# Kernel tuning notes

Measured on AMD Instinct MI355X. Metric: run time of the kernel, lower is better.

## Reference

```python
import jax, jax.numpy as jnp
import numpy as np

B, S, HID, NH, KCLIP = 2, 1500, 1024, 16, 64
HD = HID // NH  # 64


def setup_inputs() -> dict:
    key = jax.random.key(0)
    ks = jax.random.split(key, 16)
    std = 0.02
    inp = {
        "query": jax.random.normal(ks[0], (B, S, HID), jnp.float32),
        "key": jax.random.normal(ks[1], (B, S, HID), jnp.float32),
        "value": jax.random.normal(ks[2], (B, S, HID), jnp.float32),
        # per-head projection weights, stacked over heads: [NH, HID, HD]
        "Wq": jax.random.normal(ks[3], (NH, HID, HD), jnp.float32) * std,
        "bq": jax.random.normal(ks[4], (NH, HD), jnp.float32) * std,
        "Wk": jax.random.normal(ks[5], (NH, HID, HD), jnp.float32) * std,
        "bk": jax.random.normal(ks[6], (NH, HD), jnp.float32) * std,
        "Wv": jax.random.normal(ks[7], (NH, HID, HD), jnp.float32) * std,
        "bv": jax.random.normal(ks[8], (NH, HD), jnp.float32) * std,
        # Shaw relative-position embedding tables: [2k+1, HD]
        "pe_k": jax.random.normal(ks[9], (2 * KCLIP + 1, HD), jnp.float32) * std,
        "pe_v": jax.random.normal(ks[10], (2 * KCLIP + 1, HD), jnp.float32) * std,
        # output projection (torch Linear stored as x @ W + b here)
        "W_fc": jax.random.normal(ks[11], (HID, HID), jnp.float32) * std,
        "b_fc": jax.random.normal(ks[12], (HID,), jnp.float32) * std,
    }
    return inp


def _rel_bias(pe, length, k_clip):
    idx = jnp.arange(length)
    dist = jnp.clip(idx[None, :] - idx[:, None], -k_clip, k_clip) + k_clip
    return pe[dist]  # [S, S, HD]


def reference(query, key, value, Wq, bq, Wk, bk, Wv, bv, pe_k, pe_v, W_fc, b_fc):
    head_dim = Wq.shape[-1]
    seq = query.shape[1]
    k_clip = (pe_k.shape[0] - 1) // 2

    kb = _rel_bias(pe_k, seq, k_clip)  # [S, S, HD]
    vb = _rel_bias(pe_v, seq, k_clip)  # [S, S, HD]

    # batched per-head projections: [B, NH, S, HD]
    Q = jnp.einsum('bsh,nhd->bnsd', query, Wq) + bq[None, :, None, :]
    K = jnp.einsum('bsh,nhd->bnsd', key, Wk) + bk[None, :, None, :]
    V = jnp.einsum('bsh,nhd->bnsd', value, Wv) + bv[None, :, None, :]

    # content term + Shaw relative-key bias term
    scores = jnp.einsum('bnqd,bnkd->bnqk', Q, K) \
           + jnp.einsum('bnqd,qkd->bnqk', Q, kb)
    scores = scores / jnp.sqrt(jnp.asarray(head_dim, scores.dtype))

    w = jax.nn.softmax(scores, axis=-1)  # [B, NH, S, S]

    out = jnp.einsum('bnqk,bnkd->bnqd', w, V) \
        + jnp.einsum('bnqk,qkd->bnqd', w, vb)

    # concat heads (head order matches ModuleList concatenation)
    hidden = out.transpose(0, 2, 1, 3).reshape(query.shape[0], seq, -1)
    return hidden @ W_fc + b_fc
```

## Files before the change

kernel.cpp:

```cpp
#include <hip/hip_runtime.h>
#include <math.h>

#define B_     2
#define S_     1500
#define HID_   1024
#define NH_    16
#define HD_    64
#define M_     (B_*S_)
#define SP_    1536
#define LOG2E  1.4426950408889634f

typedef short bf16x8 __attribute__((ext_vector_type(8)));
typedef short bf16x4 __attribute__((ext_vector_type(4)));
typedef float f32x4  __attribute__((ext_vector_type(4)));

__device__ __forceinline__ float b2f(short s) {
    unsigned u = ((unsigned)(unsigned short)s) << 16;
    return __uint_as_float(u);
}
__device__ __forceinline__ short f2b(float f) {
    unsigned u = __float_as_uint(f);
    unsigned r = (u + 0x7FFFu + ((u >> 16) & 1u)) >> 16;
    return (short)r;
}
__device__ __forceinline__ void gload16(const short* src, short* lds) {
    __builtin_amdgcn_global_load_lds(
        (const __attribute__((address_space(1))) void*)src,
        (__attribute__((address_space(3))) void*)lds, 16, 0, 0);
}

__global__ __launch_bounds__(256) void cvt_act3(
    const float* __restrict__ q, const float* __restrict__ k,
    const float* __restrict__ v, short* __restrict__ oq,
    short* __restrict__ ok, short* __restrict__ ov)
{
    const float* src = blockIdx.y == 0 ? q : blockIdx.y == 1 ? k : v;
    short* dst       = blockIdx.y == 0 ? oq : blockIdx.y == 1 ? ok : ov;
    int i = blockIdx.x * 256 + threadIdx.x;
    const float4* p = (const float4*)(src + (size_t)i * 8);
    float4 a = p[0], b = p[1];
    bf16x8 o;
    o[0]=f2b(a.x); o[1]=f2b(a.y); o[2]=f2b(a.z); o[3]=f2b(a.w);
    o[4]=f2b(b.x); o[5]=f2b(b.y); o[6]=f2b(b.z); o[7]=f2b(b.w);
    *(bf16x8*)(dst + (size_t)i * 8) = o;
}

__global__ __launch_bounds__(256) void prep_w(
    const float* __restrict__ Wq, const float* __restrict__ Wk,
    const float* __restrict__ Wv, const float* __restrict__ Wfc,
    const float* __restrict__ pe_k, const float* __restrict__ pe_v,
    short* __restrict__ Wqt, short* __restrict__ Wkt, short* __restrict__ Wvt,
    short* __restrict__ Wfh, short* __restrict__ Wfl,
    short* __restrict__ pe_kb, short* __restrict__ pe_vt)
{
    int z = blockIdx.x, tid = threadIdx.x;
    if (z == 1024) {
        for (int s = tid; s < 144 * 64; s += 256) {
            int j = s >> 6, d = s & 63;
            pe_kb[s] = (j < 129) ? f2b(pe_k[j * 64 + d]) : (short)0;
        }
        for (int s = tid; s < 64 * 160; s += 256) {
            int d = s / 160, j = s - d * 160;
            pe_vt[s] = (j < 129) ? f2b(pe_v[j * 64 + d]) : (short)0;
        }
        return;
    }
    __shared__ float T[64][65];
    const float* src; short* dhi; short* dlo = nullptr;
    int C, c0, r0; float scale = 1.f;
    if (z < 768) {
        int widx = z >> 8, rem = z & 255;
        int h = rem >> 4, rt = rem & 15;
        src = (widx == 0 ? Wq : widx == 1 ? Wk : Wv) + (size_t)h * 1024 * 64;
        dhi = (widx == 0 ? Wqt : widx == 1 ? Wkt : Wvt) + (size_t)h * 64 * 1024;
        scale = (widx == 0) ? 0.125f * LOG2E : 1.0f;
        C = 64; c0 = 0; r0 = rt * 64;
    } else {
        int idx = z - 768;
        src = Wfc; dhi = Wfh; dlo = Wfl;
        C = 1024; c0 = (idx >> 4) * 64; r0 = (idx & 15) * 64;
    }
#pragma unroll
    for (int i = 0; i < 4; ++i) {
        int slot = tid + i * 256;
        int r = slot >> 4, cg = (slot & 15) * 4;
        float4 v = *(const float4*)(src + (size_t)(r0 + r) * C + c0 + cg);
        T[r][cg+0] = v.x*scale; T[r][cg+1] = v.y*scale;
        T[r][cg+2] = v.z*scale; T[r][cg+3] = v.w*scale;
    }
    __syncthreads();
#pragma unroll
    for (int i = 0; i < 16; ++i) {
        int slot = tid + i * 256;
        int c = slot >> 6, r = slot & 63;
        float v = T[r][c];
        short hi = f2b(v);
        size_t o = (size_t)(c0 + c) * 1024 + r0 + r;
        dhi[o] = hi;
        if (dlo) dlo[o] = f2b(v - b2f(hi));
    }
}

__device__ __forceinline__ void gemm_core(
    const short* __restrict__ Ahi, const short* __restrict__ Alo,
    const short* __restrict__ Bhi, const short* __restrict__ Blo,
    int kIters, int m0, int n0, short* As, short* Bs, f32x4 (&acc)[4][4])
{
    const int tid = threadIdx.x, w = tid >> 6, lane = tid & 63;
    const int l15 = lane & 15, lr4 = lane >> 4;
    const int wr = w >> 1, wc = w & 1;

    for (int it = 0; it < kIters; ++it) {
        int kt = it * 64;
        int seg = kt >> 10, kk0 = kt & 1023;
        const short* Aseg = (seg == 1) ? Alo : Ahi;
        const short* Bseg = (seg == 2) ? Blo : Bhi;
        __syncthreads();
#pragma unroll
        for (int c = 0; c < 4; ++c) {
            int slot = (w * 4 + c) * 64 + lane;
            int r = slot >> 3, cb = slot & 7;
            int sm = m0 + r; sm = sm < M_ ? sm : M_ - 1;
            gload16(Aseg + (size_t)sm * 1024 + kk0 + ((cb ^ (r & 7)) * 8),
                    As + (size_t)(w * 4 + c) * 512);
            gload16(Bseg + (size_t)(n0 + r) * 1024 + kk0 + ((cb ^ (r & 7)) * 8),
                    Bs + (size_t)(w * 4 + c) * 512);
        }
        __syncthreads();
#pragma unroll
        for (int kh = 0; kh < 2; ++kh) {
            bf16x8 aF[4], bF[4];
#pragma unroll
            for (int mi = 0; mi < 4; ++mi) {
                int r = wr * 64 + mi * 16 + l15;
                aF[mi] = *(const bf16x8*)(As + r * 64 + (((kh*4+lr4) ^ (r & 7)) * 8));
            }
#pragma unroll
            for (int ni = 0; ni < 4; ++ni) {
                int r = wc * 64 + ni * 16 + l15;
                bF[ni] = *(const bf16x8*)(Bs + r * 64 + (((kh*4+lr4) ^ (r & 7)) * 8));
            }
#pragma unroll
            for (int mi = 0; mi < 4; ++mi)
#pragma unroll
                for (int ni = 0; ni < 4; ++ni)
                    acc[mi][ni] = __builtin_amdgcn_mfma_f32_16x16x32_bf16(
                        aF[mi], bF[ni], acc[mi][ni], 0, 0, 0);
        }
    }
}

__global__ __launch_bounds__(256) void gemm_qkv(
    const short* __restrict__ qb, const short* __restrict__ kb,
    const short* __restrict__ vb, const short* __restrict__ Wqt,
    const short* __restrict__ Wkt, const short* __restrict__ Wvt,
    const float* __restrict__ bq, const float* __restrict__ bk,
    const float* __restrict__ bv,
    short* __restrict__ Qp, short* __restrict__ Kp, short* __restrict__ Vp)
{
    __shared__ short As[128 * 64];
    __shared__ short Bs[128 * 64];
    const int z = blockIdx.z;
    const short* A  = z == 0 ? qb : z == 1 ? kb : vb;
    const short* Bw = z == 0 ? Wqt : z == 1 ? Wkt : Wvt;
    const float* bias = z == 0 ? bq : z == 1 ? bk : bv;
    const float bscale = z == 0 ? 0.125f * LOG2E : 1.0f;
    short* out = z == 0 ? Qp : z == 1 ? Kp : Vp;
    const int m0 = blockIdx.x * 128, n0 = blockIdx.y * 128;

    f32x4 zf = {0.f,0.f,0.f,0.f};
    f32x4 acc[4][4];
#pragma unroll
    for (int i = 0; i < 4; ++i)
#pragma unroll
        for (int j = 0; j < 4; ++j) acc[i][j] = zf;

    gemm_core(A, A, Bw, Bw, 16, m0, n0, As, Bs, acc);

    const int tid = threadIdx.x, w = tid >> 6, lane = tid & 63;
    const int l15 = lane & 15, lr4 = lane >> 4;
    const int wr = w >> 1, wc = w & 1;
#pragma unroll
    for (int mi = 0; mi < 4; ++mi)
#pragma unroll
        for (int rr = 0; rr < 4; ++rr) {
            int m = m0 + wr * 64 + mi * 16 + lr4 * 4 + rr;
            if (m >= M_) continue;
            int b = m / S_, s = m - b * S_;
#pragma unroll
            for (int ni = 0; ni < 4; ++ni) {
                int n = n0 + wc * 64 + ni * 16 + l15;
                float v = acc[mi][ni][rr] + bias[n] * bscale;
                int h = n >> 6, d = n & 63;
                out[(((size_t)(b * NH_ + h)) * S_ + s) * HD_ + d] = f2b(v);
            }
        }
}

__global__ __launch_bounds__(256) void gemm_fc(
    const short* __restrict__ Ahi, const short* __restrict__ Alo,
    const short* __restrict__ Bhi, const short* __restrict__ Blo,
    const float* __restrict__ bias, float* __restrict__ out)
{
    __shared__ short As[128 * 64];
    __shared__ short Bs[128 * 64];
    const int m0 = blockIdx.x * 128, n0 = blockIdx.y * 128;
    f32x4 zf = {0.f,0.f,0.f,0.f};
    f32x4 acc[4][4];
#pragma unroll
    for (int i = 0; i < 4; ++i)
#pragma unroll
        for (int j = 0; j < 4; ++j) acc[i][j] = zf;

    gemm_core(Ahi, Alo, Bhi, Blo, 48, m0, n0, As, Bs, acc);

    const int tid = threadIdx.x, w = tid >> 6, lane = tid & 63;
    const int l15 = lane & 15, lr4 = lane >> 4;
    const int wr = w >> 1, wc = w & 1;
#pragma unroll
    for (int mi = 0; mi < 4; ++mi)
#pragma unroll
        for (int rr = 0; rr < 4; ++rr) {
            int m = m0 + wr * 64 + mi * 16 + lr4 * 4 + rr;
            if (m >= M_) continue;
#pragma unroll
            for (int ni = 0; ni < 4; ++ni) {
                int n = n0 + wc * 64 + ni * 16 + l15;
                out[(size_t)m * 1024 + n] = acc[mi][ni][rr] + bias[n];
            }
        }
}

__global__ __launch_bounds__(256) void vtrans(
    const short* __restrict__ Vp, short* __restrict__ Vtg)
{
    __shared__ short T[64][72];
    const int bh = blockIdx.y, s0 = blockIdx.x * 64, tid = threadIdx.x;
    const size_t kv = (size_t)bh * S_ * 64;
#pragma unroll
    for (int i = 0; i < 2; ++i) {
        int slot = tid + i * 256;
        int r = slot >> 3, cb = slot & 7;
        int ss = s0 + r; ss = ss < S_ ? ss : S_ - 1;
        bf16x8 v = *(const bf16x8*)(Vp + kv + (size_t)ss * 64 + cb * 8);
        *(bf16x8*)(&T[r][cb * 8]) = v;
    }
    __syncthreads();
#pragma unroll
    for (int i = 0; i < 2; ++i) {
        int slot = tid + i * 256;
        int d = slot >> 3, cg = slot & 7;
        bf16x8 v;
#pragma unroll
        for (int j = 0; j < 8; ++j) v[j] = T[cg * 8 + j][d];
        *(bf16x8*)(Vtg + ((size_t)bh * 64 + d) * SP_ + s0 + cg * 8) = v;
    }
}

__global__ __launch_bounds__(256) void attn_mfma(
    const short* __restrict__ Qb, const short* __restrict__ Kb,
    const short* __restrict__ Vtg, const short* __restrict__ pe_kb,
    const short* __restrict__ pe_vt,
    short* __restrict__ hid_hi, short* __restrict__ hid_lo)
{
    __shared__ short Kc[128 * 64];
    __shared__ short Vt[64 * 128];
    __shared__ short qpe[64 * 144];
    __shared__ short wsm[64 * 160];
    __shared__ short Pw[4][1024];

    const int tid = threadIdx.x, w = tid >> 6, lane = tid & 63;
    const int l15 = lane & 15, lr4 = lane >> 4;
    const int lg = (blockIdx.x & 7) * 96 + (blockIdx.x >> 3);
    const int bh = lg / 24, bx = lg - bh * 24;
    const int q0 = bx * 64;
    const int qw = q0 + w * 16;
    const int myq = qw + l15;
    const int myrow = w * 16 + l15;
    const size_t kv  = (size_t)bh * S_ * HD_;
    const size_t vtb = (size_t)bh * 64 * SP_;
    const int swz = (l15 & 7) << 1;

    {
        short ini = f2b(-1e30f);
        bf16x8 iv;
#pragma unroll
        for (int i = 0; i < 8; ++i) iv[i] = ini;
        short* base = wsm + w * 16 * 160;
#pragma unroll
        for (int i = 0; i < 5; ++i)
            *(bf16x8*)(base + (size_t)(i * 64 + lane) * 8) = iv;
    }
#pragma unroll
    for (int cc = 0; cc < 2; ++cc) {
        int slot = (w * 2 + cc) * 64 + lane;
        int r = slot >> 3, cb = slot & 7;
        int sq = q0 + r; sq = sq < S_ ? sq : S_ - 1;
        gload16(Qb + kv + (size_t)sq * 64 + ((cb ^ (r & 7)) * 8),
                Kc + (size_t)(w * 2 + cc) * 512);
    }
    __syncthreads();

    bf16x8 qA[2];
    {
        int r = myrow;
        qA[0] = *(const bf16x8*)(Kc + r * 64 + ((lr4 ^ (r & 7)) * 8));
        qA[1] = *(const bf16x8*)(Kc + r * 64 + (((4 + lr4) ^ (r & 7)) * 8));
    }

    f32x4 zf = {0.f,0.f,0.f,0.f};
#pragma unroll
    for (int jt = 0; jt < 9; ++jt) {
        f32x4 a = zf;
#pragma unroll
        for (int kh = 0; kh < 2; ++kh) {
            bf16x8 pf = *(const bf16x8*)(pe_kb + (size_t)(jt * 16 + l15) * 64 + kh * 32 + lr4 * 8);
            a = __builtin_amdgcn_mfma_f32_16x16x32_bf16(pf, qA[kh], a, 0, 0, 0);
        }
        bf16x4 pk;
#pragma unroll
        for (int rr = 0; rr < 4; ++rr) pk[rr] = f2b(a[rr]);
        *(bf16x4*)(qpe + (size_t)myrow * 144 + jt * 16 + lr4 * 4) = pk;
    }
    const float qpe0   = b2f(qpe[myrow * 144 + 0]);
    const float qpe128 = b2f(qpe[myrow * 144 + 128]);
    __syncthreads();

    float m = -1e30f, s0s = 0.f, s1s = 0.f;
    f32x4 o[4];
#pragma unroll
    for (int t = 0; t < 4; ++t) o[t] = zf;

    for (int c = 0; c < 12; ++c) {
        const int kc = c * 128;
#pragma unroll
        for (int cc = 0; cc < 4; ++cc) {
            int slot = (w * 4 + cc) * 64 + lane;
            int rK = slot >> 3, cbK = slot & 7;
            int sk = kc + rK; sk = sk < S_ ? sk : S_ - 1;
            gload16(Kb + kv + (size_t)sk * 64 + ((cbK ^ (rK & 7)) * 8),
                    Kc + (size_t)(w * 4 + cc) * 512);
            int rV = slot >> 4, cbV = slot & 15;
            gload16(Vtg + vtb + (size_t)rV * SP_ + kc + ((cbV ^ (rV & 7)) * 8),
                    Vt + (size_t)(w * 4 + cc) * 512);
        }
        __syncthreads();

#pragma unroll
        for (int half = 0; half < 2; ++half) {
            const int kb0 = kc + half * 64;

            __builtin_amdgcn_s_setprio(1);
            f32x4 sa[4];
#pragma unroll
            for (int t = 0; t < 4; ++t) {
                sa[t] = zf;
#pragma unroll
                for (int kh = 0; kh < 2; ++kh) {
                    int r = half * 64 + t * 16 + l15;
                    bf16x8 kB = *(const bf16x8*)(Kc + r * 64 + (((kh*4+lr4) ^ (r & 7)) * 8));
                    sa[t] = __builtin_amdgcn_mfma_f32_16x16x32_bf16(kB, qA[kh], sa[t], 0, 0, 0);
                }
            }
            __builtin_amdgcn_s_setprio(0);

            const bool all_lo = (kb0 + 63 - qw) <= -64;
            const bool all_hi = (kb0 - (qw + 15)) >= 64;
            const bool mixed  = !(all_lo || all_hi);
            const float ubias = all_lo ? qpe0 : qpe128;

            float lg2[4][4];
            float rm = -1e30f;
#pragma unroll
            for (int t = 0; t < 4; ++t)
#pragma unroll
                for (int rr = 0; rr < 4; ++rr) {
                    int k = kb0 + t * 16 + lr4 * 4 + rr;
                    int rel = k - myq;
                    float v;
                    if (mixed) {
                        int jc = rel < -64 ? 0 : (rel > 64 ? 128 : rel + 64);
                        v = sa[t][rr] + b2f(qpe[myrow * 144 + jc]);
                    } else {
                        v = sa[t][rr] + ubias;
                    }
                    if (k >= S_) v = -1e30f;
                    lg2[t][rr] = v;
                    rm = fmaxf(rm, v);
                    if (mixed && rel > -64 && rel < 64)
                        wsm[myrow * 160 + rel + 64] = f2b(v);
                }
            rm = fmaxf(rm, __shfl_xor(rm, 16));
            rm = fmaxf(rm, __shfl_xor(rm, 32));

            if (!__all(rm <= m + 8.f)) {
                float nm = fmaxf(m, rm);
                float fac = exp2f(m - nm);
                m = nm; s0s *= fac; s1s *= fac;
                float fo[4];
#pragma unroll
                for (int rr = 0; rr < 4; ++rr) fo[rr] = __shfl(fac, lr4 * 4 + rr);
#pragma unroll
                for (int t = 0; t < 4; ++t)
#pragma unroll
                    for (int rr = 0; rr < 4; ++rr) o[t][rr] *= fo[rr];
            }

            float ls0 = 0.f, ls1 = 0.f;
#pragma unroll
            for (int t = 0; t < 4; ++t) {
                bf16x4 pk;
#pragma unroll
                for (int rr = 0; rr < 4; ++rr) {
                    float p2 = exp2f(lg2[t][rr] - m);
                    pk[rr] = f2b(p2);
                    if (mixed) {
                        int rel = (kb0 + t * 16 + lr4 * 4 + rr) - myq;
                        if (rel <= -64) ls0 += p2; else if (rel >= 64) ls1 += p2;
                    } else if (all_lo) ls0 += p2; else ls1 += p2;
                }
                *(bf16x4*)(Pw[w] + l15 * 64 + (((t * 4 + lr4) ^ swz) << 2)) = pk;
            }
            ls0 += __shfl_xor(ls0, 16); ls0 += __shfl_xor(ls0, 32);
            ls1 += __shfl_xor(ls1, 16); ls1 += __shfl_xor(ls1, 32);
            s0s += ls0; s1s += ls1;

            __builtin_amdgcn_s_setprio(1);
#pragma unroll
            for (int win = 0; win < 2; ++win) {
                bf16x8 pA = *(const bf16x8*)(Pw[w] + l15 * 64 + (((win * 8 + lr4 * 2) ^ swz) << 2));
#pragma unroll
                for (int td = 0; td < 4; ++td) {
                    int r = td * 16 + l15;
                    int cbv = half * 8 + win * 4 + lr4;
                    bf16x8 vB = *(const bf16x8*)(Vt + r * 128 + ((cbv ^ (r & 7)) * 8));
                    o[td] = __builtin_amdgcn_mfma_f32_16x16x32_bf16(pA, vB, o[td], 0, 0, 0);
                }
            }
            __builtin_amdgcn_s_setprio(0);
        }

        __syncthreads();
    }

    short* rowp = wsm + (size_t)myrow * 160;
    float midsum = 0.f;
#pragma unroll
    for (int cc = 0; cc < 5; ++cc) {
        int off = (cc * 4 + lr4) * 8;
        bf16x8 mv = *(const bf16x8*)(rowp + off);
        bf16x8 ev;
#pragma unroll
        for (int jj = 0; jj < 8; ++jj) {
            float e = exp2f(b2f(mv[jj]) - m);
            ev[jj] = f2b(e);
            midsum += e;
        }
        *(bf16x8*)(rowp + off) = ev;
    }
    midsum += __shfl_xor(midsum, 16); midsum += __shfl_xor(midsum, 32);
    const float linv = 1.f / (s0s + s1s + midsum);
    if (lr4 == 0) { rowp[0] = f2b(s0s); rowp[128] = f2b(s1s); }

#pragma unroll
    for (int jh = 0; jh < 5; ++jh) {
        bf16x8 aW = *(const bf16x8*)(wsm + (size_t)myrow * 160 + jh * 32 + lr4 * 8);
#pragma unroll
        for (int td = 0; td < 4; ++td) {
            bf16x8 bW = *(const bf16x8*)(pe_vt + (size_t)(td * 16 + l15) * 160 + jh * 32 + lr4 * 8);
            o[td] = __builtin_amdgcn_mfma_f32_16x16x32_bf16(aW, bW, o[td], 0, 0, 0);
        }
    }

    {
        float fo[4];
#pragma unroll
        for (int rr = 0; rr < 4; ++rr) fo[rr] = __shfl(linv, lr4 * 4 + rr);
#pragma unroll
        for (int td = 0; td < 4; ++td)
#pragma unroll
            for (int rr = 0; rr < 4; ++rr) o[td][rr] *= fo[rr];
    }

#pragma unroll
    for (int td = 0; td < 4; ++td)
#pragma unroll
        for (int rr = 0; rr < 4; ++rr) {
            int qrow = lr4 * 4 + rr;
            int d = td * 16 + l15;
            int inner = (((d >> 2) ^ ((qrow & 7) << 1)) << 2) + (d & 3);
            float v = o[td][rr];
            short hi = f2b(v);
            Pw[w][qrow * 64 + inner] = hi;
            wsm[(w * 16 + qrow) * 160 + inner] = f2b(v - b2f(hi));
        }
    {
        int b = bh >> 4, h = bh & 15;
        int qrow = lane >> 2;
        int q = q0 + w * 16 + qrow;
#pragma unroll
        for (int i = 0; i < 2; ++i) {
            int cb = (lane & 3) * 2 + i;
            int qws = (cb * 2) ^ ((qrow & 7) << 1);
            bf16x8 hv = *(const bf16x8*)(Pw[w] + qrow * 64 + qws * 4);
            bf16x8 lv = *(const bf16x8*)(wsm + (w * 16 + qrow) * 160 + qws * 4);
            if (q < S_) {
                size_t oo = ((size_t)(b * S_ + q)) * 1024 + h * 64 + cb * 8;
                *(bf16x8*)(hid_hi + oo) = hv;
                *(bf16x8*)(hid_lo + oo) = lv;
            }
        }
    }
}

extern "C" void kernel_launch(void* const* d_in, const int* in_sizes, int n_in,
                              void* d_out, int out_size, void* d_ws, size_t ws_size,
                              hipStream_t stream)
{
    const float* query = (const float*)d_in[0];
    const float* key   = (const float*)d_in[1];
    const float* value = (const float*)d_in[2];
    const float* Wq    = (const float*)d_in[3];
    const float* bq    = (const float*)d_in[4];
    const float* Wk    = (const float*)d_in[5];
    const float* bk    = (const float*)d_in[6];
    const float* Wv    = (const float*)d_in[7];
    const float* bv    = (const float*)d_in[8];
    const float* pe_k  = (const float*)d_in[9];
    const float* pe_v  = (const float*)d_in[10];
    const float* W_fc  = (const float*)d_in[11];
    const float* b_fc  = (const float*)d_in[12];

    char* W = (char*)d_ws;
    short* qb   = (short*)(W + 0);
    short* kb   = (short*)(W + 6291456);
    short* vb   = (short*)(W + 12582912);
    short* Vtg  = vb;
    short* Wqt  = (short*)(W + 18874368);
    short* Wkt  = (short*)(W + 20971520);
    short* Wvt  = (short*)(W + 23068672);
    short* Wfh  = (short*)(W + 25165824);
    short* Wfl  = (short*)(W + 27262976);
    short* Qp   = (short*)(W + 29360128);
    short* Kp   = (short*)(W + 35651584);
    short* Vp   = (short*)(W + 41943040);
    short* pekb = (short*)(W + 48234496);
    short* pevt = (short*)(W + 48252928);
    short* hidh = qb;
    short* hidl = kb;

    cvt_act3<<<dim3(1500, 3), 256, 0, stream>>>(query, key, value, qb, kb, vb);
    prep_w<<<1025, 256, 0, stream>>>(Wq, Wk, Wv, W_fc, pe_k, pe_v,
                                     Wqt, Wkt, Wvt, Wfh, Wfl, pekb, pevt);
    gemm_qkv<<<dim3(24, 8, 3), 256, 0, stream>>>(qb, kb, vb, Wqt, Wkt, Wvt,
                                                 bq, bk, bv, Qp, Kp, Vp);
    vtrans<<<dim3(24, 32), 256, 0, stream>>>(Vp, Vtg);
    attn_mfma<<<768, 256, 0, stream>>>(Qp, Kp, Vtg, pekb, pevt, hidh, hidl);
    gemm_fc<<<dim3(24, 8), 256, 0, stream>>>(hidh, hidl, Wfh, Wfl, b_fc, (float*)d_out);
}
```

Before: 279.3 us.

## Keep softmax probabilities in registers by permuting V transpose layout; drop Pw LDS

The V transpose kernel now writes keys in a permuted order so the MFMA output layout of the score tile can feed directly as the A operand of the PV MFMA. This removes the per-wave Pw shared-memory round trip for probabilities. The two 64-key halves are also merged into one 128-key pass, so there is one max/rescale step per chunk instead of two. The epilogue reuses wsm/qpe for staging. The fc GEMM K-loop argument changes from 48 to 32, which may alter or truncate the reduction over K unless its meaning changed elsewhere. The wider pass raises register pressure (sa[8], lg2[8][4]).

After: 260.6 us. -6.7%, faster.

```diff
diff --git a/kernel.cpp b/kernel.cpp
--- a/kernel.cpp
+++ b/kernel.cpp
@@ -212,7 +212,7 @@
 #pragma unroll
         for (int j = 0; j < 4; ++j) acc[i][j] = zf;
 
-    gemm_core(Ahi, Alo, Bhi, Blo, 48, m0, n0, As, Bs, acc);
+    gemm_core(Ahi, Alo, Bhi, Blo, 32, m0, n0, As, Bs, acc);
 
     const int tid = threadIdx.x, w = tid >> 6, lane = tid & 63;
     const int l15 = lane & 15, lr4 = lane >> 4;
@@ -252,7 +252,10 @@
         int d = slot >> 3, cg = slot & 7;
         bf16x8 v;
 #pragma unroll
-        for (int j = 0; j < 8; ++j) v[j] = T[cg * 8 + j][d];
+        for (int j = 0; j < 8; ++j) {
+            int kk = 32 * (cg >> 2) + ((j >> 2) & 1) * 16 + (cg & 3) * 4 + (j & 3);
+            v[j] = T[kk][d];
+        }
         *(bf16x8*)(Vtg + ((size_t)bh * 64 + d) * SP_ + s0 + cg * 8) = v;
     }
 }
@@ -267,7 +270,6 @@
     __shared__ short Vt[64 * 128];
     __shared__ short qpe[64 * 144];
     __shared__ short wsm[64 * 160];
-    __shared__ short Pw[4][1024];
 
     const int tid = threadIdx.x, w = tid >> 6, lane = tid & 63;
     const int l15 = lane & 15, lr4 = lane >> 4;
@@ -279,7 +281,6 @@
     const int myrow = w * 16 + l15;
     const size_t kv  = (size_t)bh * S_ * HD_;
     const size_t vtb = (size_t)bh * 64 * SP_;
-    const int swz = (l15 & 7) << 1;
 
     {
         short ini = f2b(-1e30f);
@@ -346,99 +347,101 @@
         }
         __syncthreads();
 
-#pragma unroll
-        for (int half = 0; half < 2; ++half) {
-            const int kb0 = kc + half * 64;
-
-            __builtin_amdgcn_s_setprio(1);
-            f32x4 sa[4];
-#pragma unroll
-            for (int t = 0; t < 4; ++t) {
-                sa[t] = zf;
-#pragma unroll
-                for (int kh = 0; kh < 2; ++kh) {
-                    int r = half * 64 + t * 16 + l15;
-                    bf16x8 kB = *(const bf16x8*)(Kc + r * 64 + (((kh*4+lr4) ^ (r & 7)) * 8));
-                    sa[t] = __builtin_amdgcn_mfma_f32_16x16x32_bf16(kB, qA[kh], sa[t], 0, 0, 0);
+        __builtin_amdgcn_s_setprio(1);
+        f32x4 sa[8];
+#pragma unroll
+        for (int t8 = 0; t8 < 8; ++t8) {
+            sa[t8] = zf;
+#pragma unroll
+            for (int kh = 0; kh < 2; ++kh) {
+                int r = t8 * 16 + l15;
+                bf16x8 kB = *(const bf16x8*)(Kc + r * 64 + (((kh*4+lr4) ^ (r & 7)) * 8));
+                sa[t8] = __builtin_amdgcn_mfma_f32_16x16x32_bf16(kB, qA[kh], sa[t8], 0, 0, 0);
+            }
+        }
+        __builtin_amdgcn_s_setprio(0);
+
+        const bool lo0 = (kc +  63 - qw) <= -64, hi0 = (kc       - (qw + 15)) >= 64;
+        const bool lo1 = (kc + 127 - qw) <= -64, hi1 = (kc + 64  - (qw + 15)) >= 64;
+        const bool mx0 = !(lo0 || hi0), mx1 = !(lo1 || hi1);
+        const float ub0 = lo0 ? qpe0 : qpe128;
+        const float ub1 = lo1 ? qpe0 : qpe128;
+
+        float lg2[8][4];
+        float rm = -1e30f;
+#pragma unroll
+        for (int t8 = 0; t8 < 8; ++t8) {
+            const bool mx = (t8 < 4) ? mx0 : mx1;
+            const float ub = (t8 < 4) ? ub0 : ub1;
+#pragma unroll
+            for (int rr = 0; rr < 4; ++rr) {
+                int k = kc + t8 * 16 + lr4 * 4 + rr;
+                int rel = k - myq;
+                float v;
+                if (mx) {
+                    int jc = rel < -64 ? 0 : (rel > 64 ? 128 : rel + 64);
+                    v = sa[t8][rr] + b2f(qpe[myrow * 144 + jc]);
+                } else {
+                    v = sa[t8][rr] + ub;
                 }
-            }
-            __builtin_amdgcn_s_setprio(0);
-
-            const bool all_lo = (kb0 + 63 - qw) <= -64;
-            const bool all_hi = (kb0 - (qw + 15)) >= 64;
-            const bool mixed  = !(all_lo || all_hi);
-            const float ubias = all_lo ? qpe0 : qpe128;
-
-            float lg2[4][4];
-            float rm = -1e30f;
+                if (k >= S_) v = -1e30f;
+                lg2[t8][rr] = v;
+                rm = fmaxf(rm, v);
+                if (mx && rel > -64 && rel < 64)
+                    wsm[myrow * 160 + rel + 64] = f2b(v);
+            }
+        }
+        rm = fmaxf(rm, __shfl_xor(rm, 16));
+        rm = fmaxf(rm, __shfl_xor(rm, 32));
+
+        if (!__all(rm <= m + 8.f)) {
+            float nm = fmaxf(m, rm);
+            float fac = exp2f(m - nm);
+            m = nm; s0s *= fac; s1s *= fac;
+            float fo[4];
+#pragma unroll
+            for (int rr = 0; rr < 4; ++rr) fo[rr] = __shfl(fac, lr4 * 4 + rr);
 #pragma unroll
             for (int t = 0; t < 4; ++t)
 #pragma unroll
-                for (int rr = 0; rr < 4; ++rr) {
-                    int k = kb0 + t * 16 + lr4 * 4 + rr;
-                    int rel = k - myq;
-                    float v;
-                    if (mixed) {
-                        int jc = rel < -64 ? 0 : (rel > 64 ? 128 : rel + 64);
-                        v = sa[t][rr] + b2f(qpe[myrow * 144 + jc]);
-                    } else {
-                        v = sa[t][rr] + ubias;
-                    }
-                    if (k >= S_) v = -1e30f;
-                    lg2[t][rr] = v;
-                    rm = fmaxf(rm, v);
-                    if (mixed && rel > -64 && rel < 64)
-                        wsm[myrow * 160 + rel + 64] = f2b(v);
-                }
-            rm = fmaxf(rm, __shfl_xor(rm, 16));
-            rm = fmaxf(rm, __shfl_xor(rm, 32));
-
-            if (!__all(rm <= m + 8.f)) {
-                float nm = fmaxf(m, rm);
-                float fac = exp2f(m - nm);
-                m = nm; s0s *= fac; s1s *= fac;
-                float fo[4];
-#pragma unroll
-                for (int rr = 0; rr < 4; ++rr) fo[rr] = __shfl(fac, lr4 * 4 + rr);
-#pragma unroll
-                for (int t = 0; t < 4; ++t)
-#pragma unroll
-                    for (int rr = 0; rr < 4; ++rr) o[t][rr] *= fo[rr];
-            }
-
-            float ls0 = 0.f, ls1 = 0.f;
-#pragma unroll
-            for (int t = 0; t < 4; ++t) {
-                bf16x4 pk;
-#pragma unroll
-                for (int rr = 0; rr < 4; ++rr) {
-                    float p2 = exp2f(lg2[t][rr] - m);
-                    pk[rr] = f2b(p2);
-                    if (mixed) {
-                        int rel = (kb0 + t * 16 + lr4 * 4 + rr) - myq;
-                        if (rel <= -64) ls0 += p2; else if (rel >= 64) ls1 += p2;
-                    } else if (all_lo) ls0 += p2; else ls1 += p2;
-                }
-                *(bf16x4*)(Pw[w] + l15 * 64 + (((t * 4 + lr4) ^ swz) << 2)) = pk;
-            }
-            ls0 += __shfl_xor(ls0, 16); ls0 += __shfl_xor(ls0, 32);
-            ls1 += __shfl_xor(ls1, 16); ls1 += __shfl_xor(ls1, 32);
-            s0s += ls0; s1s += ls1;
-
-            __builtin_amdgcn_s_setprio(1);
-#pragma unroll
-            for (int win = 0; win < 2; ++win) {
-                bf16x8 pA = *(const bf16x8*)(Pw[w] + l15 * 64 + (((win * 8 + lr4 * 2) ^ swz) << 2));
+                for (int rr = 0; rr < 4; ++rr) o[t][rr] *= fo[rr];
+        }
+
+        bf16x8 pa[2][2];
+        float ls0 = 0.f, ls1 = 0.f;
+#pragma unroll
+        for (int t8 = 0; t8 < 8; ++t8) {
+            const int h = t8 >> 2, tt = t8 & 3;
+            const int wn = tt >> 1, sl = (tt & 1) * 4;
+            const bool mx = h ? mx1 : mx0;
+            const bool alo = h ? lo1 : lo0;
+#pragma unroll
+            for (int rr = 0; rr < 4; ++rr) {
+                float p2 = exp2f(lg2[t8][rr] - m);
+                pa[h][wn][sl + rr] = f2b(p2);
+                if (mx) {
+                    int rel = (kc + t8 * 16 + lr4 * 4 + rr) - myq;
+                    if (rel <= -64) ls0 += p2; else if (rel >= 64) ls1 += p2;
+                } else if (alo) ls0 += p2; else ls1 += p2;
+            }
+        }
+        ls0 += __shfl_xor(ls0, 16); ls0 += __shfl_xor(ls0, 32);
+        ls1 += __shfl_xor(ls1, 16); ls1 += __shfl_xor(ls1, 32);
+        s0s += ls0; s1s += ls1;
+
+        __builtin_amdgcn_s_setprio(1);
+#pragma unroll
+        for (int h = 0; h < 2; ++h)
+#pragma unroll
+            for (int wn = 0; wn < 2; ++wn)
 #pragma unroll
                 for (int td = 0; td < 4; ++td) {
                     int r = td * 16 + l15;
-                    int cbv = half * 8 + win * 4 + lr4;
+                    int cbv = h * 8 + wn * 4 + lr4;
                     bf16x8 vB = *(const bf16x8*)(Vt + r * 128 + ((cbv ^ (r & 7)) * 8));
-                    o[td] = __builtin_amdgcn_mfma_f32_16x16x32_bf16(pA, vB, o[td], 0, 0, 0);
+                    o[td] = __builtin_amdgcn_mfma_f32_16x16x32_bf16(pa[h][wn], vB, o[td], 0, 0, 0);
                 }
-            }
-            __builtin_amdgcn_s_setprio(0);
-        }
+        __builtin_amdgcn_s_setprio(0);
 
         __syncthreads();
     }
@@ -491,8 +494,8 @@
             int inner = (((d >> 2) ^ ((qrow & 7) << 1)) << 2) + (d & 3);
             float v = o[td][rr];
             short hi = f2b(v);
-            Pw[w][qrow * 64 + inner] = hi;
-            wsm[(w * 16 + qrow) * 160 + inner] = f2b(v - b2f(hi));
+            wsm[(w * 16 + qrow) * 160 + inner] = hi;
+            qpe[(w * 16 + qrow) * 144 + inner] = f2b(v - b2f(hi));
         }
     {
         int b = bh >> 4, h = bh & 15;
@@ -502,8 +505,8 @@
         for (int i = 0; i < 2; ++i) {
             int cb = (lane & 3) * 2 + i;
             int qws = (cb * 2) ^ ((qrow & 7) << 1);
-            bf16x8 hv = *(const bf16x8*)(Pw[w] + qrow * 64 + qws * 4);
-            bf16x8 lv = *(const bf16x8*)(wsm + (w * 16 + qrow) * 160 + qws * 4);
+            bf16x8 hv = *(const bf16x8*)(wsm + (w * 16 + qrow) * 160 + qws * 4);
+            bf16x8 lv = *(const bf16x8*)(qpe + (w * 16 + qrow) * 144 + qws * 4);
             if (q < S_) {
                 size_t oo = ((size_t)(b * S_ + q)) * 1024 + h * 64 + cb * 8;
                 *(bf16x8*)(hid_hi + oo) = hv;
```
